# Performance work log

Hardware: AMD Instinct MI355X
Metric: run time of the kernel (lower is better)

The kernel has to match this reference:

```python
import jax, jax.numpy as jnp
import numpy as np

H, L, N = 1024, 2048, 32
EPS = 1e-7


def _hippo_lambda(n):
    # make_NPLR_HiPPO(2n) -> eigenvalues of skew part, keep first n with imag>0, shift by -0.5
    i = np.arange(2 * n, dtype=np.float64)
    x = 2 * i + 1
    hippo = np.tril(np.sqrt(np.outer(x, x)), k=-1)
    skew = (hippo - hippo.T) / 2
    lam = np.linalg.eig(skew)[0]
    idx = np.nonzero(lam.imag > 0)[0][:n]
    lam_sel = lam[idx] - 0.5
    return np.stack([lam_sel.real, lam_sel.imag], -1).astype(np.float32)


def setup_inputs() -> dict:
    key = jax.random.key(0)
    k1, k2, k3 = jax.random.split(key, 3)
    u = jax.random.normal(k1, (H, L), dtype=jnp.float32)
    # lecun-style scale for W (fan_in ~ N)
    W = jax.random.normal(k2, (H, N, 2), dtype=jnp.float32) / np.float32(np.sqrt(N))
    # log_step_initializer(dt_min=1e-3, dt_max=0.1)
    log_step = jax.random.uniform(k3, (H,), dtype=jnp.float32) * np.float32(np.log(0.1) - np.log(1e-3)) + np.float32(np.log(1e-3))
    Lambda_ri = jnp.asarray(_hippo_lambda(N))
    D = jnp.ones((H,), dtype=jnp.float32)
    return {"u": u, "W": W, "Lambda_ri": Lambda_ri, "log_step": log_step, "D": D}


def _complex_softmax(x):
    # softmax over complex vector, stabilized by the entry with max real part
    x2 = x - x[jnp.argmax(x.real)]
    e = jnp.exp(x2)
    s = jnp.sum(e)
    return e * (s.conj() / (s * s.conj() + EPS))


def _dss_kernel(Wc, Lam, step, length):
    # P: (N, L) complex; kernel = (W / Lambda) @ complex_softmax_rows(P)
    P = (step * Lam)[:, None] * jnp.arange(length)
    S = jax.vmap(_complex_softmax)(P)
    return ((Wc / Lam) @ S).real  # (L,)


def _fft_conv(u, K):
    # non-circular convolution via zero-padded rfft of length 2L
    n = u.shape[0]
    ud = jnp.fft.rfft(jnp.pad(u, (0, n)))
    Kd = jnp.fft.rfft(jnp.pad(K, (0, n)))
    return jnp.fft.irfft(ud * Kd)[:n]


def reference(u, W, Lambda_ri, log_step, D):
    Lam = Lambda_ri[:, 0] + 1j * Lambda_ri[:, 1]  # shared HiPPO eigenvalues (N,)
    Wc = W[..., 0] + 1j * W[..., 1]               # (H, N) complex
    step = jnp.exp(log_step)                      # (H,)

    def per_channel(u_h, W_h, step_h, D_h):
        K = _dss_kernel(W_h, Lam, step_h, u_h.shape[0])
        return _fft_conv(u_h, K) + D_h * u_h

    return jax.vmap(per_channel)(u, Wc, step, D)
```

## Files before the change

kernel.cpp:

```cpp
#include <hip/hip_runtime.h>
#include <math.h>


static constexpr int kH = 1024;
static constexpr int kL = 2048;
static constexpr int kN = 32;
static constexpr int kChunk = 32;
static constexpr int kNChunk = kL / kChunk;
static constexpr double kEps = 1e-7;

__global__ void dss_setup_kernel(const float* __restrict__ W,
                                 const float* __restrict__ Lambda_ri,
                                 const float* __restrict__ log_step,
                                 float* __restrict__ zc) {
    int idx = blockIdx.x * blockDim.x + threadIdx.x;
    if (idx >= kH * kN) return;
    int h = idx / kN;
    int n = idx % kN;

    double step = exp((double)log_step[h]);
    double lr = (double)Lambda_ri[2 * n + 0];
    double li = (double)Lambda_ri[2 * n + 1];
    double wr = (double)W[(h * kN + n) * 2 + 0];
    double wi = (double)W[(h * kN + n) * 2 + 1];

    double ar = step * lr;
    double ai = step * li;

    double er = exp(ar);
    double zr = er * cos(ai);
    double zi = er * sin(ai);

    double eL = exp(ar * (double)kL);
    double thL = ai * (double)kL;
    double zLr = eL * cos(thL);
    double zLi = eL * sin(thL);

    double nr = 1.0 - zLr, ni = -zLi;
    double dr = 1.0 - zr,  di = -zi;
    double dd = dr * dr + di * di;
    double sr = (nr * dr + ni * di) / dd;
    double si = (ni * dr - nr * di) / dd;

    double ll = lr * lr + li * li;
    double qr = (wr * lr + wi * li) / ll;
    double qi = (wi * lr - wr * li) / ll;

    double ss = sr * sr + si * si + kEps;
    double cr = (qr * sr + qi * si) / ss;
    double ci = (qi * sr - qr * si) / ss;

    double eC = exp(ar * (double)kChunk);
    double thC = ai * (double)kChunk;
    double zCr = eC * cos(thC);
    double zCi = eC * sin(thC);

    float* o = zc + idx * 8;
    o[0] = (float)zr;  o[1] = (float)zi;
    o[2] = (float)cr;  o[3] = (float)ci;
    o[4] = (float)zCr; o[5] = (float)zCi;
    o[6] = 0.f;        o[7] = 0.f;
}

__launch_bounds__(64, 1)
__global__ void dss_scan_kernel(const float* __restrict__ u,
                                const float* __restrict__ zc,
                                const float* __restrict__ Dv,
                                float* __restrict__ y) {
    __shared__ float u_s[kL + kL / 32];
    __shared__ float eR[kNChunk][kN + 1];
    __shared__ float eI[kNChunk][kN + 1];

    const int h = blockIdx.x;
    const int t = threadIdx.x;

    const float* uh = u + (size_t)h * kL;
    for (int i = t; i < kL; i += 64) {
        u_s[i + (i >> 5)] = uh[i];
    }

    const float* zch = zc + (size_t)h * kN * 8;
    float z_r[kN], z_i[kN], c_r[kN], c_i[kN];
#pragma unroll
    for (int n = 0; n < kN; ++n) {
        z_r[n] = zch[n * 8 + 0];
        z_i[n] = zch[n * 8 + 1];
        c_r[n] = zch[n * 8 + 2];
        c_i[n] = zch[n * 8 + 3];
    }
    __syncthreads();

    float x_r[kN], x_i[kN];
#pragma unroll
    for (int n = 0; n < kN; ++n) { x_r[n] = 0.f; x_i[n] = 0.f; }

    const int base = t * kChunk;
    for (int k = 0; k < kChunk; ++k) {
        const int i = base + k;
        const float uv = u_s[i + (i >> 5)];
#pragma unroll
        for (int n = 0; n < kN; ++n) {
            const float tr = z_i[n] * x_r[n];
            x_r[n] = fmaf(z_r[n], x_r[n], fmaf(-z_i[n], x_i[n], uv));
            x_i[n] = fmaf(z_r[n], x_i[n], tr);
        }
    }
#pragma unroll
    for (int n = 0; n < kN; ++n) { eR[t][n] = x_r[n]; eI[t][n] = x_i[n]; }
    __syncthreads();

    if (t < kN) {
        const int n = t;
        const float zCr = zch[n * 8 + 4];
        const float zCi = zch[n * 8 + 5];
        float Er = 0.f, Ei = 0.f;
        for (int j = 0; j < kNChunk; ++j) {
            const float ejr = eR[j][n];
            const float eji = eI[j][n];
            eR[j][n] = Er;
            eI[j][n] = Ei;
            const float nr2 = fmaf(zCr, Er, fmaf(-zCi, Ei, ejr));
            const float ni2 = fmaf(zCr, Ei, fmaf(zCi, Er, eji));
            Er = nr2; Ei = ni2;
        }
    }
    __syncthreads();

    const float Dh = Dv[h];
#pragma unroll
    for (int n = 0; n < kN; ++n) { x_r[n] = eR[t][n]; x_i[n] = eI[t][n]; }

    for (int k = 0; k < kChunk; ++k) {
        const int i = base + k;
        const float uv = u_s[i + (i >> 5)];
        float acc = Dh * uv;
#pragma unroll
        for (int n = 0; n < kN; ++n) {
            const float tr = z_i[n] * x_r[n];
            x_r[n] = fmaf(z_r[n], x_r[n], fmaf(-z_i[n], x_i[n], uv));
            x_i[n] = fmaf(z_r[n], x_i[n], tr);
            acc = fmaf(c_r[n], x_r[n], acc);
            acc = fmaf(-c_i[n], x_i[n], acc);
        }
        u_s[i + (i >> 5)] = acc;
    }
    __syncthreads();

    float* yh = y + (size_t)h * kL;
    for (int i = t; i < kL; i += 64) {
        yh[i] = u_s[i + (i >> 5)];
    }
}

extern "C" void kernel_launch(void* const* d_in, const int* in_sizes, int n_in,
                              void* d_out, int out_size, void* d_ws, size_t ws_size,
                              hipStream_t stream) {
    const float* u        = (const float*)d_in[0];
    const float* W        = (const float*)d_in[1];
    const float* Lam      = (const float*)d_in[2];
    const float* log_step = (const float*)d_in[3];
    const float* Dv       = (const float*)d_in[4];
    float* y = (float*)d_out;
    float* zc = (float*)d_ws;

    dss_setup_kernel<<<(kH * kN + 255) / 256, 256, 0, stream>>>(W, Lam, log_step, zc);
    dss_scan_kernel<<<kH, 64, 0, stream>>>(u, zc, Dv, y);
}
```

Measured before the change: 98.68 us.

## Split state modes across two waves and replace serial chunk carry with shuffle scan

The scan kernel now uses 128 threads per channel, with each wave owning 16 of the 32 state modes. This halves per-thread register state and work, and partial outputs are summed through two shared buffers. The serial 64-step inter-chunk carry done by 32 threads is replaced by a log-depth wave-level shuffle scan with repeated squaring of the chunk multiplier. The setup kernel moves from double to float math and uses expm1/sin-half-angle for a stable denominator, trading some precision for cheaper arithmetic.

```diff
diff --git a/kernel.cpp b/kernel.cpp
--- a/kernel.cpp
+++ b/kernel.cpp
@@ -6,8 +6,8 @@
 static constexpr int kL = 2048;
 static constexpr int kN = 32;
 static constexpr int kChunk = 32;
-static constexpr int kNChunk = kL / kChunk;
-static constexpr double kEps = 1e-7;
+static constexpr int kMpW = 16;
+static constexpr float kEps = 1e-7f;
 
 __global__ void dss_setup_kernel(const float* __restrict__ W,
                                  const float* __restrict__ Lambda_ri,
@@ -18,137 +18,155 @@
     int h = idx / kN;
     int n = idx % kN;
 
-    double step = exp((double)log_step[h]);
-    double lr = (double)Lambda_ri[2 * n + 0];
-    double li = (double)Lambda_ri[2 * n + 1];
-    double wr = (double)W[(h * kN + n) * 2 + 0];
-    double wi = (double)W[(h * kN + n) * 2 + 1];
+    float step = expf(log_step[h]);
+    float lr = Lambda_ri[2 * n + 0];
+    float li = Lambda_ri[2 * n + 1];
+    float wr = W[(h * kN + n) * 2 + 0];
+    float wi = W[(h * kN + n) * 2 + 1];
 
-    double ar = step * lr;
-    double ai = step * li;
+    float ar = step * lr;
+    float ai = step * li;
 
-    double er = exp(ar);
-    double zr = er * cos(ai);
-    double zi = er * sin(ai);
+    float ea = expf(ar);
+    float sb, cb;
+    sincosf(ai, &sb, &cb);
+    float zr = ea * cb, zi = ea * sb;
 
-    double eL = exp(ar * (double)kL);
-    double thL = ai * (double)kL;
-    double zLr = eL * cos(thL);
-    double zLi = eL * sin(thL);
+    float em = expm1f(ar);
+    float sh = sinf(0.5f * ai);
+    float dr = fmaf(-em, cb, 2.f * sh * sh);
+    float di = -ea * sb;
 
-    double nr = 1.0 - zLr, ni = -zLi;
-    double dr = 1.0 - zr,  di = -zi;
-    double dd = dr * dr + di * di;
-    double sr = (nr * dr + ni * di) / dd;
-    double si = (ni * dr - nr * di) / dd;
+    float eL = expf(ar * (float)kL);
+    float sL, cL;
+    sincosf(ai * (float)kL, &sL, &cL);
+    float nr = 1.f - eL * cL;
+    float ni = -eL * sL;
 
-    double ll = lr * lr + li * li;
-    double qr = (wr * lr + wi * li) / ll;
-    double qi = (wi * lr - wr * li) / ll;
+    float dd = dr * dr + di * di;
+    float id = 1.f / dd;
+    float sr = (nr * dr + ni * di) * id;
+    float si = (ni * dr - nr * di) * id;
 
-    double ss = sr * sr + si * si + kEps;
-    double cr = (qr * sr + qi * si) / ss;
-    double ci = (qi * sr - qr * si) / ss;
+    float ll = lr * lr + li * li;
+    float il = 1.f / ll;
+    float qr = (wr * lr + wi * li) * il;
+    float qi = (wi * lr - wr * li) * il;
 
-    double eC = exp(ar * (double)kChunk);
-    double thC = ai * (double)kChunk;
-    double zCr = eC * cos(thC);
-    double zCi = eC * sin(thC);
+    float ss = fmaf(sr, sr, fmaf(si, si, kEps));
+    float is = 1.f / ss;
+    float cr = (qr * sr + qi * si) * is;
+    float ci = (qi * sr - qr * si) * is;
+
+    float eC = expf(ar * (float)kChunk);
+    float sC, cC;
+    sincosf(ai * (float)kChunk, &sC, &cC);
 
     float* o = zc + idx * 8;
-    o[0] = (float)zr;  o[1] = (float)zi;
-    o[2] = (float)cr;  o[3] = (float)ci;
-    o[4] = (float)zCr; o[5] = (float)zCi;
-    o[6] = 0.f;        o[7] = 0.f;
+    o[0] = zr;      o[1] = zi;
+    o[2] = cr;      o[3] = ci;
+    o[4] = eC * cC; o[5] = eC * sC;
+    o[6] = 0.f;     o[7] = 0.f;
 }
 
-__launch_bounds__(64, 1)
-__global__ void dss_scan_kernel(const float* __restrict__ u,
-                                const float* __restrict__ zc,
-                                const float* __restrict__ Dv,
-                                float* __restrict__ y) {
-    __shared__ float u_s[kL + kL / 32];
-    __shared__ float eR[kNChunk][kN + 1];
-    __shared__ float eI[kNChunk][kN + 1];
+__global__ __launch_bounds__(128, 2)
+void dss_scan_kernel(const float* __restrict__ u,
+                     const float* __restrict__ zc,
+                     const float* __restrict__ Dv,
+                     float* __restrict__ y) {
+    __shared__ float u_s[kL + (kL >> 5)];
+    __shared__ float y0_s[kL + (kL >> 5)];
+    __shared__ float y1_s[kL + (kL >> 5)];
 
     const int h = blockIdx.x;
-    const int t = threadIdx.x;
+    const int tid = threadIdx.x;
+    const int wave = tid >> 6;
+    const int lane = tid & 63;
 
     const float* uh = u + (size_t)h * kL;
-    for (int i = t; i < kL; i += 64) {
-        u_s[i + (i >> 5)] = uh[i];
-    }
+    for (int i = tid; i < kL; i += 128) u_s[i + (i >> 5)] = uh[i];
 
-    const float* zch = zc + (size_t)h * kN * 8;
-    float z_r[kN], z_i[kN], c_r[kN], c_i[kN];
+    const float* zch = zc + ((size_t)h * kN + wave * kMpW) * 8;
+    float zr[kMpW], zi[kMpW], cr[kMpW], ci[kMpW];
 #pragma unroll
-    for (int n = 0; n < kN; ++n) {
-        z_r[n] = zch[n * 8 + 0];
-        z_i[n] = zch[n * 8 + 1];
-        c_r[n] = zch[n * 8 + 2];
-        c_i[n] = zch[n * 8 + 3];
+    for (int n = 0; n < kMpW; ++n) {
+        zr[n] = zch[n * 8 + 0];
+        zi[n] = zch[n * 8 + 1];
+        cr[n] = zch[n * 8 + 2];
+        ci[n] = zch[n * 8 + 3];
     }
     __syncthreads();
 
-    float x_r[kN], x_i[kN];
+    float er[kMpW], ei[kMpW];
 #pragma unroll
-    for (int n = 0; n < kN; ++n) { x_r[n] = 0.f; x_i[n] = 0.f; }
+    for (int n = 0; n < kMpW; ++n) { er[n] = 0.f; ei[n] = 0.f; }
 
-    const int base = t * kChunk;
+    const int base = lane * kChunk;
     for (int k = 0; k < kChunk; ++k) {
         const int i = base + k;
         const float uv = u_s[i + (i >> 5)];
 #pragma unroll
-        for (int n = 0; n < kN; ++n) {
-            const float tr = z_i[n] * x_r[n];
-            x_r[n] = fmaf(z_r[n], x_r[n], fmaf(-z_i[n], x_i[n], uv));
-            x_i[n] = fmaf(z_r[n], x_i[n], tr);
+        for (int n = 0; n < kMpW; ++n) {
+            const float tr = zi[n] * er[n];
+            er[n] = fmaf(zr[n], er[n], fmaf(-zi[n], ei[n], uv));
+            ei[n] = fmaf(zr[n], ei[n], tr);
         }
     }
+
 #pragma unroll
-    for (int n = 0; n < kN; ++n) { eR[t][n] = x_r[n]; eI[t][n] = x_i[n]; }
-    __syncthreads();
+    for (int n = 0; n < kMpW; ++n) {
+        float vr = __shfl_up(er[n], 1);
+        float vi = __shfl_up(ei[n], 1);
+        er[n] = (lane >= 1) ? vr : 0.f;
+        ei[n] = (lane >= 1) ? vi : 0.f;
+    }
+    float pr[kMpW], pi[kMpW];
+#pragma unroll
+    for (int n = 0; n < kMpW; ++n) { pr[n] = zch[n * 8 + 4]; pi[n] = zch[n * 8 + 5]; }
 
-    if (t < kN) {
-        const int n = t;
-        const float zCr = zch[n * 8 + 4];
-        const float zCi = zch[n * 8 + 5];
-        float Er = 0.f, Ei = 0.f;
-        for (int j = 0; j < kNChunk; ++j) {
-            const float ejr = eR[j][n];
-            const float eji = eI[j][n];
-            eR[j][n] = Er;
-            eI[j][n] = Ei;
-            const float nr2 = fmaf(zCr, Er, fmaf(-zCi, Ei, ejr));
-            const float ni2 = fmaf(zCr, Ei, fmaf(zCi, Er, eji));
-            Er = nr2; Ei = ni2;
+#pragma unroll
+    for (int d = 1; d < 64; d <<= 1) {
+#pragma unroll
+        for (int n = 0; n < kMpW; ++n) {
+            float vr = __shfl_up(er[n], d);
+            float vi = __shfl_up(ei[n], d);
+            const bool ok = (lane >= d);
+            vr = ok ? vr : 0.f;
+            vi = ok ? vi : 0.f;
+            er[n] = fmaf(pr[n], vr, fmaf(-pi[n], vi, er[n]));
+            ei[n] = fmaf(pr[n], vi, fmaf(pi[n], vr, ei[n]));
+        }
+        if (d < 32) {
+#pragma unroll
+            for (int n = 0; n < kMpW; ++n) {
+                const float t = fmaf(pr[n], pr[n], -pi[n] * pi[n]);
+                pi[n] = 2.f * pr[n] * pi[n];
+                pr[n] = t;
+            }
         }
     }
-    __syncthreads();
 
     const float Dh = Dv[h];
-#pragma unroll
-    for (int n = 0; n < kN; ++n) { x_r[n] = eR[t][n]; x_i[n] = eI[t][n]; }
-
+    float* ys = wave ? y1_s : y0_s;
     for (int k = 0; k < kChunk; ++k) {
         const int i = base + k;
         const float uv = u_s[i + (i >> 5)];
-        float acc = Dh * uv;
+        float acc = wave ? 0.f : Dh * uv;
 #pragma unroll
-        for (int n = 0; n < kN; ++n) {
-            const float tr = z_i[n] * x_r[n];
-            x_r[n] = fmaf(z_r[n], x_r[n], fmaf(-z_i[n], x_i[n], uv));
-            x_i[n] = fmaf(z_r[n], x_i[n], tr);
-            acc = fmaf(c_r[n], x_r[n], acc);
-            acc = fmaf(-c_i[n], x_i[n], acc);
+        for (int n = 0; n < kMpW; ++n) {
+            const float tr = zi[n] * er[n];
+            er[n] = fmaf(zr[n], er[n], fmaf(-zi[n], ei[n], uv));
+            ei[n] = fmaf(zr[n], ei[n], tr);
+            acc = fmaf(cr[n], er[n], acc);
+            acc = fmaf(-ci[n], ei[n], acc);
         }
-        u_s[i + (i >> 5)] = acc;
+        ys[i + (i >> 5)] = acc;
     }
     __syncthreads();
 
     float* yh = y + (size_t)h * kL;
-    for (int i = t; i < kL; i += 64) {
-        yh[i] = u_s[i + (i >> 5)];
+    for (int i = tid; i < kL; i += 128) {
+        yh[i] = y0_s[i + (i >> 5)] + y1_s[i + (i >> 5)];
     }
 }
 
@@ -160,9 +178,9 @@
     const float* Lam      = (const float*)d_in[2];
     const float* log_step = (const float*)d_in[3];
     const float* Dv       = (const float*)d_in[4];
-    float* y = (float*)d_out;
+    float* y  = (float*)d_out;
     float* zc = (float*)d_ws;
 
     dss_setup_kernel<<<(kH * kN + 255) / 256, 256, 0, stream>>>(W, Lam, log_step, zc);
-    dss_scan_kernel<<<kH, 64, 0, stream>>>(u, zc, Dv, y);
+    dss_scan_kernel<<<kH, 128, 0, stream>>>(u, zc, Dv, y);
 }
```

New measurement: 89.72 us. 1.1x faster.
